# Optimization experiments

Hardware: AMD Instinct MI355X
Metric: run time of the kernel (lower is better)

The kernel has to match this reference:

```python
import jax, jax.numpy as jnp
import numpy as np

BSZ, L, H, P = 8, 4096, 512, 256  # batch, seq len, features, complex state dim (conj_sym)
DT_MIN, DT_MAX = 1e-3, 1e-1


def setup_inputs() -> dict:
    key = jax.random.key(0)
    k_u, k_B, k_C, k_D, k_dt = jax.random.split(key, 5)
    u = jax.random.normal(k_u, (BSZ, L, H), dtype=jnp.float32)
    # HiPPO-like stable init for the diagonal state matrix
    Lambda_re = -0.5 * jnp.ones((P,), dtype=jnp.float32)
    Lambda_im = jnp.pi * jnp.arange(P, dtype=jnp.float32)
    # lecun-normal-ish scaling for real/imag parts of B (fan_in = H) and C (fan_in = P)
    B = jax.random.normal(k_B, (P, H, 2), dtype=jnp.float32) / jnp.sqrt(2.0 * H)
    C = jax.random.normal(k_C, (H, P, 2), dtype=jnp.float32) / jnp.sqrt(2.0 * P)
    D = jax.random.normal(k_D, (H,), dtype=jnp.float32)
    log_step = jax.random.uniform(k_dt, (P, 1), dtype=jnp.float32,
                                  minval=jnp.log(DT_MIN), maxval=jnp.log(DT_MAX))
    return {"u": u, "Lambda_re": Lambda_re, "Lambda_im": Lambda_im,
            "B": B, "C": C, "D": D, "log_step": log_step}


def _binop(q_i, q_j):
    """Associative binary operator for diagonal linear recurrence."""
    A_i, b_i = q_i
    A_j, b_j = q_j
    return (A_j * A_i, A_j * b_i + b_j)


def reference(u, Lambda_re, Lambda_im, B, C, D, log_step):
    # --- setup / discretization (zero-order hold) ---
    Lambda = (Lambda_re + 1j * Lambda_im).astype(jnp.complex64)      # (P,)
    B_tilde = (B[..., 0] + 1j * B[..., 1]).astype(jnp.complex64)     # (P,H)
    C_tilde = (C[..., 0] + 1j * C[..., 1]).astype(jnp.complex64)     # (H,P)
    step = jnp.exp(log_step[:, 0])                                   # (P,)
    Lambda_bar = jnp.exp(Lambda * step)                              # (P,)
    B_bar = ((Lambda_bar - 1.0) / Lambda)[:, None] * B_tilde         # (P,H)

    # --- parallel scan over the sequence (diagonal SSM) ---
    Bu = jnp.einsum('blh,ph->blp', u, B_bar)                         # (B,L,P) complex64
    Lam = jnp.broadcast_to(Lambda_bar, Bu.shape)                     # (B,L,P)
    _, xs = jax.lax.associative_scan(_binop, (Lam, Bu), axis=1)      # (B,L,P)

    # --- emissions (factor 2 from conjugate symmetry) + feedthrough ---
    ys = 2.0 * jnp.einsum('blp,hp->blh', xs, C_tilde).real + D * u   # (B,L,H)
    return jax.nn.gelu(ys)
```

## Files before the change

### kernel.cpp

```cpp
#include <hip/hip_runtime.h>
#include <cstdint>
#include <cstddef>

typedef unsigned short u16;
typedef short short8 __attribute__((ext_vector_type(8)));
typedef float floatx4 __attribute__((ext_vector_type(4)));

#define DEVINL __device__ __forceinline__

static constexpr int BSZ = 8, SEQL = 4096, H = 512, P = 256;
static constexpr int M = BSZ * SEQL;
static constexpr int KD = 512;
static constexpr int ND = 512;
static constexpr int CHUNK = 64;
static constexpr int NCH = SEQL / CHUNK;

DEVINL u16 f2bf(float f) {
  union { float f; unsigned u; } v; v.f = f;
  unsigned r = (v.u + 0x7fffu + ((v.u >> 16) & 1u)) >> 16;
  return (u16)r;
}
DEVINL float bf2f(u16 h) {
  union { unsigned u; float f; } v; v.u = ((unsigned)h) << 16; return v.f;
}

__global__ void setup_kernel(const float* __restrict__ Lre, const float* __restrict__ Lim,
                             const float* __restrict__ logstep,
                             float2* __restrict__ lam, float2* __restrict__ ffac) {
  int p = threadIdx.x;
  if (p >= P) return;
  float lr = Lre[p], li = Lim[p];
  float st = expf(logstep[p]);
  float mag = expf(lr * st);
  float ang = li * st;
  float cr = mag * cosf(ang);
  float ci = mag * sinf(ang);
  lam[p] = make_float2(cr, ci);
  float a = cr - 1.0f, b = ci;
  float den = lr * lr + li * li;
  float fr = (a * lr + b * li) / den;
  float fi = (b * lr - a * li) / den;
  ffac[p] = make_float2(fr, fi);
}

__global__ void bt1_kernel(const float2* __restrict__ Bin,
                           const float2* __restrict__ ffac,
                           u16* __restrict__ bt1) {
  int idx = blockIdx.x * 256 + threadIdx.x;
  int p = idx / H, h = idx % H;
  float2 bv = Bin[(size_t)p * H + h];
  float2 f = ffac[p];
  float br = f.x * bv.x - f.y * bv.y;
  float bi = f.x * bv.y + f.y * bv.x;
  bt1[(size_t)(2 * p) * H + h]     = f2bf(br);
  bt1[(size_t)(2 * p + 1) * H + h] = f2bf(bi);
}

__global__ void bt2_kernel(const float* __restrict__ Cin, u16* __restrict__ bt2) {
  int idx = blockIdx.x * 256 + threadIdx.x;
  float c = Cin[idx];
  float v = (idx & 1) ? -2.0f * c : 2.0f * c;
  bt2[idx] = f2bf(v);
}

__global__ void ucvt_kernel(const float4* __restrict__ uin, ushort4* __restrict__ ubf) {
  int idx = blockIdx.x * 256 + threadIdx.x;
  float4 f = uin[idx];
  ushort4 o;
  o.x = f2bf(f.x); o.y = f2bf(f.y); o.z = f2bf(f.z); o.w = f2bf(f.w);
  ubf[idx] = o;
}

template <int MODE>
__global__ __launch_bounds__(256, 2) void gemm_bt(const u16* __restrict__ A,
                                                  const u16* __restrict__ Bt,
                                                  u16* __restrict__ outBf,
                                                  float* __restrict__ outF,
                                                  const float* __restrict__ Dv,
                                                  const float* __restrict__ u32) {
  constexpr int LDSS = 40;
  __shared__ u16 As[128 * LDSS];
  __shared__ u16 Bs[128 * LDSS];
  const int tid = threadIdx.x;
  const int bm = blockIdx.x, bn = blockIdx.y;
  const int wave = tid >> 6, lane = tid & 63;
  const int quad = lane >> 4, l16 = lane & 15;
  const int wm = (wave & 1) << 6, wn = (wave >> 1) << 6;

  floatx4 acc[4][4] = {};

  const u16* Ab = A + (size_t)bm * 128 * KD;
  const u16* Bb = Bt + (size_t)bn * 128 * KD;
  const int lrow = tid >> 2;
  const int lcol = (tid & 3) << 3;

  for (int k0 = 0; k0 < KD; k0 += 32) {
    __syncthreads();
    *(short8*)&As[lrow * LDSS + lcol] =
        *(const short8*)&Ab[(size_t)lrow * KD + k0 + lcol];
    *(short8*)&As[(lrow + 64) * LDSS + lcol] =
        *(const short8*)&Ab[(size_t)(lrow + 64) * KD + k0 + lcol];
    *(short8*)&Bs[lrow * LDSS + lcol] =
        *(const short8*)&Bb[(size_t)lrow * KD + k0 + lcol];
    *(short8*)&Bs[(lrow + 64) * LDSS + lcol] =
        *(const short8*)&Bb[(size_t)(lrow + 64) * KD + k0 + lcol];
    __syncthreads();

    short8 af[4], bf[4];
#pragma unroll
    for (int t = 0; t < 4; t++)
      af[t] = *(const short8*)&As[(wm + t * 16 + l16) * LDSS + quad * 8];
#pragma unroll
    for (int t = 0; t < 4; t++)
      bf[t] = *(const short8*)&Bs[(wn + t * 16 + l16) * LDSS + quad * 8];
#pragma unroll
    for (int tm = 0; tm < 4; tm++)
#pragma unroll
      for (int tn = 0; tn < 4; tn++)
        acc[tm][tn] = __builtin_amdgcn_mfma_f32_16x16x32_bf16(af[tm], bf[tn], acc[tm][tn], 0, 0, 0);
  }

  const int row_base = bm * 128 + wm + quad * 4;
  const int col_base = bn * 128 + wn + l16;
#pragma unroll
  for (int tm = 0; tm < 4; tm++) {
#pragma unroll
    for (int tn = 0; tn < 4; tn++) {
      int n = col_base + tn * 16;
#pragma unroll
      for (int r = 0; r < 4; r++) {
        int m = row_base + tm * 16 + r;
        float v = acc[tm][tn][r];
        if (MODE == 0) {
          outBf[(size_t)m * ND + n] = f2bf(v);
        } else {
          float ys = v + Dv[n] * u32[(size_t)m * ND + n];
          float y3 = ys * ys * ys;
          float t = tanhf(0.7978845608028654f * (ys + 0.044715f * y3));
          outF[(size_t)m * ND + n] = 0.5f * ys * (1.0f + t);
        }
      }
    }
  }
}

__global__ __launch_bounds__(256) void scan_carry(const u16* __restrict__ Bu,
                                                  const float2* __restrict__ lam,
                                                  float2* __restrict__ carry) {
  int p = threadIdx.x;
  int c = blockIdx.x;
  int b = blockIdx.y;
  float2 lm = lam[p];
  float xr = 0.f, xi = 0.f;
  const u16* base = Bu + ((size_t)b * SEQL + (size_t)c * CHUNK) * 512 + 2 * p;
  for (int l = 0; l < CHUNK; l++) {
    unsigned w = *(const unsigned*)(base + (size_t)l * 512);
    float br = bf2f((u16)(w & 0xffffu));
    float bi = bf2f((u16)(w >> 16));
    float nr = lm.x * xr - lm.y * xi + br;
    float ni = lm.x * xi + lm.y * xr + bi;
    xr = nr; xi = ni;
  }
  carry[((size_t)b * NCH + c) * P + p] = make_float2(xr, xi);
}

__global__ __launch_bounds__(256) void scan_prefix(const float2* __restrict__ carry,
                                                   const float2* __restrict__ lam,
                                                   float2* __restrict__ prefix) {
  int p = threadIdx.x;
  int b = blockIdx.x;
  float2 lm = lam[p];
  float ar = lm.x, ai = lm.y;
  for (int i = 0; i < 6; i++) { float nr = ar * ar - ai * ai, ni = 2.f * ar * ai; ar = nr; ai = ni; }
  float pr = 0.f, pi = 0.f;
  for (int c = 0; c < NCH; c++) {
    prefix[((size_t)b * NCH + c) * P + p] = make_float2(pr, pi);
    float2 ca = carry[((size_t)b * NCH + c) * P + p];
    float nr = ar * pr - ai * pi + ca.x;
    float ni = ar * pi + ai * pr + ca.y;
    pr = nr; pi = ni;
  }
}

__global__ __launch_bounds__(256) void scan_apply(u16* __restrict__ Bu,
                                                  const float2* __restrict__ lam,
                                                  const float2* __restrict__ prefix) {
  int p = threadIdx.x;
  int c = blockIdx.x;
  int b = blockIdx.y;
  float2 lm = lam[p];
  float2 pf = prefix[((size_t)b * NCH + c) * P + p];
  float xr = pf.x, xi = pf.y;
  u16* base = Bu + ((size_t)b * SEQL + (size_t)c * CHUNK) * 512 + 2 * p;
  for (int l = 0; l < CHUNK; l++) {
    unsigned* addr = (unsigned*)(base + (size_t)l * 512);
    unsigned w = *addr;
    float br = bf2f((u16)(w & 0xffffu));
    float bi = bf2f((u16)(w >> 16));
    float nr = lm.x * xr - lm.y * xi + br;
    float ni = lm.x * xi + lm.y * xr + bi;
    xr = nr; xi = ni;
    *addr = (unsigned)f2bf(nr) | ((unsigned)f2bf(ni) << 16);
  }
}

extern "C" void kernel_launch(void* const* d_in, const int* in_sizes, int n_in,
                              void* d_out, int out_size, void* d_ws, size_t ws_size,
                              hipStream_t stream) {
  const float* u      = (const float*)d_in[0];
  const float* Lre    = (const float*)d_in[1];
  const float* Lim    = (const float*)d_in[2];
  const float* Bin    = (const float*)d_in[3];
  const float* Cin    = (const float*)d_in[4];
  const float* Dv     = (const float*)d_in[5];
  const float* lstep  = (const float*)d_in[6];
  float* out          = (float*)d_out;

  char* ws = (char*)d_ws;
  float2* lam    = (float2*)(ws + 0);
  float2* ffac   = (float2*)(ws + 2048);
  u16*    bt1    = (u16*)   (ws + 4096);
  u16*    bt2    = (u16*)   (ws + 528384);
  u16*    ubf    = (u16*)   (ws + 1052672);
  u16*    Bu     = (u16*)   (ws + 34607104);
  float2* carry  = (float2*)(ws + 68161536);
  float2* prefix = (float2*)(ws + 69210112);

  setup_kernel<<<1, 256, 0, stream>>>(Lre, Lim, lstep, lam, ffac);
  bt1_kernel<<<(P * H) / 256, 256, 0, stream>>>((const float2*)Bin, ffac, bt1);
  bt2_kernel<<<(H * P * 2) / 256, 256, 0, stream>>>(Cin, bt2);
  ucvt_kernel<<<(M * H / 4) / 256, 256, 0, stream>>>((const float4*)u, (ushort4*)ubf);

  gemm_bt<0><<<dim3(M / 128, ND / 128), 256, 0, stream>>>(ubf, bt1, Bu, nullptr, nullptr, nullptr);

  scan_carry <<<dim3(NCH, BSZ), 256, 0, stream>>>(Bu, lam, carry);
  scan_prefix<<<BSZ, 256, 0, stream>>>(carry, lam, prefix);
  scan_apply <<<dim3(NCH, BSZ), 256, 0, stream>>>(Bu, lam, prefix);

  gemm_bt<1><<<dim3(M / 128, ND / 128), 256, 0, stream>>>(Bu, bt2, nullptr, out, Dv, u);
}
```

Baseline: 227.4 us.

## Use direct global-to-LDS loads in GEMM and read bf16 u in epilogue

```diff
diff --git a/kernel.cpp b/kernel.cpp
--- a/kernel.cpp
+++ b/kernel.cpp
@@ -22,6 +22,12 @@
 }
 DEVINL float bf2f(u16 h) {
   union { unsigned u; float f; } v; v.u = ((unsigned)h) << 16; return v.f;
+}
+
+DEVINL void gload_lds16(const u16* g, u16* l) {
+  __builtin_amdgcn_global_load_lds(
+      (const __attribute__((address_space(1))) unsigned*)g,
+      (__attribute__((address_space(3))) unsigned*)l, 16, 0, 0);
 }
 
 __global__ void setup_kernel(const float* __restrict__ Lre, const float* __restrict__ Lim,
@@ -72,15 +78,14 @@
 }
 
 template <int MODE>
-__global__ __launch_bounds__(256, 2) void gemm_bt(const u16* __restrict__ A,
+__global__ __launch_bounds__(256, 4) void gemm_bt(const u16* __restrict__ A,
                                                   const u16* __restrict__ Bt,
                                                   u16* __restrict__ outBf,
                                                   float* __restrict__ outF,
                                                   const float* __restrict__ Dv,
-                                                  const float* __restrict__ u32) {
-  constexpr int LDSS = 40;
-  __shared__ u16 As[128 * LDSS];
-  __shared__ u16 Bs[128 * LDSS];
+                                                  const u16* __restrict__ ubf) {
+  __shared__ u16 As[128 * 32];
+  __shared__ u16 Bs[128 * 32];
   const int tid = threadIdx.x;
   const int bm = blockIdx.x, bn = blockIdx.y;
   const int wave = tid >> 6, lane = tid & 63;
@@ -91,28 +96,24 @@
 
   const u16* Ab = A + (size_t)bm * 128 * KD;
   const u16* Bb = Bt + (size_t)bn * 128 * KD;
-  const int lrow = tid >> 2;
-  const int lcol = (tid & 3) << 3;
+  const int srow = tid >> 2;
+  const int scol = (tid & 3) << 3;
 
   for (int k0 = 0; k0 < KD; k0 += 32) {
     __syncthreads();
-    *(short8*)&As[lrow * LDSS + lcol] =
-        *(const short8*)&Ab[(size_t)lrow * KD + k0 + lcol];
-    *(short8*)&As[(lrow + 64) * LDSS + lcol] =
-        *(const short8*)&Ab[(size_t)(lrow + 64) * KD + k0 + lcol];
-    *(short8*)&Bs[lrow * LDSS + lcol] =
-        *(const short8*)&Bb[(size_t)lrow * KD + k0 + lcol];
-    *(short8*)&Bs[(lrow + 64) * LDSS + lcol] =
-        *(const short8*)&Bb[(size_t)(lrow + 64) * KD + k0 + lcol];
+    gload_lds16(Ab + (size_t)srow * KD + k0 + scol,        &As[tid * 8]);
+    gload_lds16(Ab + (size_t)(srow + 64) * KD + k0 + scol, &As[2048 + tid * 8]);
+    gload_lds16(Bb + (size_t)srow * KD + k0 + scol,        &Bs[tid * 8]);
+    gload_lds16(Bb + (size_t)(srow + 64) * KD + k0 + scol, &Bs[2048 + tid * 8]);
     __syncthreads();
 
     short8 af[4], bf[4];
 #pragma unroll
     for (int t = 0; t < 4; t++)
-      af[t] = *(const short8*)&As[(wm + t * 16 + l16) * LDSS + quad * 8];
+      af[t] = *(const short8*)&As[(wm + t * 16 + l16) * 32 + quad * 8];
 #pragma unroll
     for (int t = 0; t < 4; t++)
-      bf[t] = *(const short8*)&Bs[(wn + t * 16 + l16) * LDSS + quad * 8];
+      bf[t] = *(const short8*)&Bs[(wn + t * 16 + l16) * 32 + quad * 8];
 #pragma unroll
     for (int tm = 0; tm < 4; tm++)
 #pragma unroll
@@ -122,6 +123,11 @@
 
   const int row_base = bm * 128 + wm + quad * 4;
   const int col_base = bn * 128 + wn + l16;
+  float dv[4];
+  if (MODE == 1) {
+#pragma unroll
+    for (int tn = 0; tn < 4; tn++) dv[tn] = Dv[col_base + tn * 16];
+  }
 #pragma unroll
   for (int tm = 0; tm < 4; tm++) {
 #pragma unroll
@@ -134,7 +140,8 @@
         if (MODE == 0) {
           outBf[(size_t)m * ND + n] = f2bf(v);
         } else {
-          float ys = v + Dv[n] * u32[(size_t)m * ND + n];
+          float uv = bf2f(ubf[(size_t)m * ND + n]);
+          float ys = v + dv[tn] * uv;
           float y3 = ys * ys * ys;
           float t = tanhf(0.7978845608028654f * (ys + 0.044715f * y3));
           outF[(size_t)m * ND + n] = 0.5f * ys * (1.0f + t);
@@ -237,5 +244,5 @@
   scan_prefix<<<BSZ, 256, 0, stream>>>(carry, lam, prefix);
   scan_apply <<<dim3(NCH, BSZ), 256, 0, stream>>>(Bu, lam, prefix);
 
-  gemm_bt<1><<<dim3(M / 128, ND / 128), 256, 0, stream>>>(Bu, bt2, nullptr, out, Dv, u);
-}
+  gemm_bt<1><<<dim3(M / 128, ND / 128), 256, 0, stream>>>(Bu, bt2, nullptr, out, Dv, ubf);
+}
```

Result: faster. 217.3 us (-4.4%).
